# Kernel tuning notes

Hardware: AMD Instinct MI355X
Metric: run time of the kernel (lower is better)

## Reference

```python
import jax, jax.numpy as jnp
import numpy as np
import math
from jax import lax


def _conv(x, w, b, stride=1, pad=0, groups=1):
    # x: [B,C,H,W], w: [O, C//groups, kh, kw] (OIHW)
    out = lax.conv_general_dilated(x, w, (stride, stride), [(pad, pad), (pad, pad)],
                                   feature_group_count=groups,
                                   dimension_numbers=('NCHW', 'OIHW', 'NCHW'))
    return out + b.reshape(1, -1, 1, 1)


def _shared_conv(x, k2d, b, stride=1, pad=0):
    # SharedConv: one [k,k] kernel shared across all channels (depthwise), scalar bias
    C = x.shape[1]
    w = jnp.broadcast_to(k2d[None, None], (C, 1) + k2d.shape)
    out = lax.conv_general_dilated(x, w, (stride, stride), [(pad, pad), (pad, pad)],
                                   feature_group_count=C,
                                   dimension_numbers=('NCHW', 'OIHW', 'NCHW'))
    return out + b


def _bn(x, g, b, m, v, eps=1e-5):
    scale = (g / jnp.sqrt(v + eps)).reshape(1, -1, 1, 1)
    return (x - m.reshape(1, -1, 1, 1)) * scale + b.reshape(1, -1, 1, 1)


def _leaky(x, s=0.01):
    return jnp.where(x >= 0, x, s * x)


def _max_leaky(x, t, s):
    # cap values above threshold with leaky slope
    return jnp.where(x <= t, x, t + s * (x - t))


def _min_leaky(x, t, s):
    # cap values below threshold with leaky slope
    return jnp.where(x >= t, x, t + s * (x - t))


def _mode_pool(x, k=11, padding=1):
    # histogram mode pooling: 17 bins over quantized values, stride 1
    xp = jnp.pad(x, ((0, 0), (0, 0), (padding, padding), (padding, padding)))
    bins = jnp.clip(jnp.round(xp * 16.0), 0.0, 16.0).astype(jnp.int32)
    oh = jax.nn.one_hot(bins, 17, dtype=x.dtype)           # [B,C,Hp,Wp,17]
    counts = lax.reduce_window(oh, 0.0, lax.add, (1, 1, k, k, 1), (1, 1, 1, 1, 1), 'VALID')
    return jnp.argmax(counts, axis=-1).astype(x.dtype) / 16.0


def _emphase(x, w, k=11):
    # EmphaseLocal: unsharp-style local emphasis with per-channel learnable scale
    s = lax.reduce_window(x, 0.0, lax.add, (1, 1, k, k), (1, 1, 1, 1), 'SAME')
    avg = s / float(k * k)
    return x + w.reshape(1, -1, 1, 1) * (x - avg)


def setup_inputs() -> dict:
    key = jax.random.key(0)
    ks = jax.random.split(key, 20)
    f32 = jnp.float32
    B, Cin, H, W = 2, 3, 512, 512
    C2 = 64  # half_out_channels * 2
    return {
        'x': jax.random.uniform(ks[0], (B, Cin, H, W), f32),
        'w1': jax.random.normal(ks[1], (C2, Cin, 1, 1), f32) * 0.1,
        'b1': jax.random.normal(ks[2], (C2,), f32) * 0.05,
        'w2': jax.random.normal(ks[3], (C2, 2, 1, 1), f32) * 0.1,  # groups=32
        'b2': jax.random.normal(ks[4], (C2,), f32) * 0.05,
        'down_k': jax.random.normal(ks[5], (3, 3), f32) * 0.1,
        'down_b': jax.random.normal(ks[6], (), f32) * 0.05,
        'ft_gamma': 1.0 + jax.random.normal(ks[7], (C2,), f32) * 0.1,
        'ft_beta': jax.random.normal(ks[8], (C2,), f32) * 0.05,
        'ft_mean': jax.random.normal(ks[9], (C2,), f32) * 0.05,
        'ft_var': jax.random.uniform(ks[10], (C2,), f32, 0.5, 1.5),
        'ft_k': jax.random.normal(ks[11], (1, 1), f32) * 0.5 + 1.0,
        'ft_b': jax.random.normal(ks[12], (), f32) * 0.05,
        'emph_w': jax.random.normal(ks[13], (C2,), f32) * 0.1,
        'interp_k': jax.random.normal(ks[14], (5, 5), f32) * 0.1,
        'interp_b': jax.random.normal(ks[15], (), f32) * 0.05,
        'i_gamma': 1.0 + jax.random.normal(ks[16], (C2,), f32) * 0.1,
        'i_beta': jax.random.normal(ks[17], (C2,), f32) * 0.05,
        'i_mean': jax.random.normal(ks[18], (C2,), f32) * 0.05,
        'i_var': jax.random.uniform(ks[19], (C2,), f32, 0.5, 1.5),
    }


def reference(x, w1, b1, w2, b2, down_k, down_b,
              ft_gamma, ft_beta, ft_mean, ft_var, ft_k, ft_b, emph_w,
              interp_k, interp_b, i_gamma, i_beta, i_mean, i_var):
    B, _, H, W = x.shape
    C2 = w1.shape[0]
    # prepare: ColorDownsample(16) -> ModePool2d(11,1,1) -> 1x1 conv -> MaxLeakyReLU -> grouped 1x1 conv -> MinLeakyReLU
    xd = jnp.round(x * 255.0 / 16.0) * 16.0 / 256.0
    h = _mode_pool(xd, k=11, padding=1)                 # [B,Cin,H-8,W-8]
    h = _max_leaky(_conv(h, w1, b1), 0.1, 0.01)
    groups = C2 // w2.shape[1]
    d = _min_leaky(_conv(h, w2, b2, groups=groups), 0.1, 0.01)
    score = jnp.zeros((B, C2, H, W), x.dtype)
    n = math.floor(math.log(min(d.shape[2], d.shape[3]), 3))
    for _ in range(n):
        # downgrade: shared 3x3 stride-3 conv + leaky
        d = _leaky(_shared_conv(d, down_k, down_b, stride=3, pad=1))
        # zoom back to full resolution, then interpolate branch (shared 5x5 conv + BN + leaky)
        z = jax.image.resize(d, (B, C2, H, W), method='bilinear')
        z = _bn(_shared_conv(z, interp_k, interp_b, pad=2), i_gamma, i_beta, i_mean, i_var)
        score = score + _leaky(z)
    # ft applied 3 times with shared weights: BN -> shared 1x1 conv -> EmphaseLocal
    for _ in range(3):
        s = _bn(score, ft_gamma, ft_beta, ft_mean, ft_var)
        s = _shared_conv(s, ft_k, ft_b)
        score = _emphase(s, emph_w, k=11)
    return score
```

## Files before the change

### kernel.cpp

```cpp
#include <hip/hip_runtime.h>

#define NB 2
#define CIN 3
#define HH 512
#define WW 512
#define C2 64
#define HM 504

typedef float v2f  __attribute__((ext_vector_type(2)));
typedef float v2fu __attribute__((ext_vector_type(2), aligned(4)));

__global__ __launch_bounds__(256) void k_mode(const float* __restrict__ x,
                                              unsigned char* __restrict__ hmode) {
  __shared__ unsigned char tile[26 * 26];
  int bc  = blockIdx.z;
  int ty0 = blockIdx.y * 16, tx0 = blockIdx.x * 16;
  const float* src = x + (size_t)bc * HH * WW;
  for (int i = threadIdx.x; i < 26 * 26; i += 256) {
    int r = i / 26, cl = i % 26;
    int Y = ty0 + r, X = tx0 + cl;
    unsigned char v = 0;
    if (Y >= 1 && Y <= HH && X >= 1 && X <= WW) {
      float val = src[(Y - 1) * WW + (X - 1)];
      float q = rintf((val * 255.0f) / 16.0f);
      q = fminf(fmaxf(q, 0.0f), 16.0f);
      v = (unsigned char)(int)q;
    }
    tile[i] = v;
  }
  __syncthreads();
  int ty = threadIdx.x >> 4, tx = threadIdx.x & 15;
  int oy = ty0 + ty, ox = tx0 + tx;
  if (oy >= HM || ox >= HM) return;
  unsigned long long w0 = 0, w1 = 0, w2 = 0;
  for (int dy = 0; dy < 11; dy++) {
    #pragma unroll
    for (int dx = 0; dx < 11; dx++) {
      int b = tile[(ty + dy) * 26 + tx + dx];
      unsigned long long inc = 1ull << ((b & 7) * 8);
      if (b < 8) w0 += inc;
      else if (b < 16) w1 += inc;
      else w2 += inc;
    }
  }
  int best = -1, bestb = 0;
  #pragma unroll
  for (int b = 0; b < 17; b++) {
    int cnt;
    if (b < 8)       cnt = (int)((w0 >> (b * 8)) & 0xff);
    else if (b < 16) cnt = (int)((w1 >> ((b - 8) * 8)) & 0xff);
    else             cnt = (int)(w2 & 0xff);
    if (cnt > best) { best = cnt; bestb = b; }
  }
  hmode[bc * HM * HM + oy * HM + ox] = (unsigned char)bestb;
}

__global__ __launch_bounds__(256) void k_prepare(const unsigned char* __restrict__ hmode,
                                                 const float* __restrict__ w1,
                                                 const float* __restrict__ b1,
                                                 const float* __restrict__ w2,
                                                 const float* __restrict__ b2,
                                                 const float* __restrict__ down_k,
                                                 const float* __restrict__ down_b,
                                                 float* __restrict__ d1) {
  int bc = blockIdx.y;
  int b  = bc >> 6;
  int c  = bc & 63;
  int pix = blockIdx.x * 256 + threadIdx.x;
  if (pix >= 168 * 168) return;
  int oy = pix / 168, ox = pix % 168;
  int c0 = (c >> 1) << 1;
  float w1a0 = w1[c0 * 3], w1a1 = w1[c0 * 3 + 1], w1a2 = w1[c0 * 3 + 2], b1a = b1[c0];
  float w1b0 = w1[(c0 + 1) * 3], w1b1 = w1[(c0 + 1) * 3 + 1], w1b2 = w1[(c0 + 1) * 3 + 2], b1b = b1[c0 + 1];
  float w2a = w2[c * 2], w2b = w2[c * 2 + 1], b2c = b2[c];
  float kb = *down_b;
  const unsigned char* h0p = hmode + (b * 3 + 0) * HM * HM;
  const unsigned char* h1p = hmode + (b * 3 + 1) * HM * HM;
  const unsigned char* h2p = hmode + (b * 3 + 2) * HM * HM;
  float acc = 0.0f;
  #pragma unroll
  for (int ky = 0; ky < 3; ky++) {
    int y = 3 * oy - 1 + ky;
    if (y < 0 || y >= HM) continue;
    #pragma unroll
    for (int kx = 0; kx < 3; kx++) {
      int xx = 3 * ox - 1 + kx;
      if (xx < 0 || xx >= HM) continue;
      int o = y * HM + xx;
      float hh0 = h0p[o] * (1.0f / 16.0f);
      float hh1 = h1p[o] * (1.0f / 16.0f);
      float hh2 = h2p[o] * (1.0f / 16.0f);
      float a0 = w1a0 * hh0 + w1a1 * hh1 + w1a2 * hh2 + b1a;
      float a1 = w1b0 * hh0 + w1b1 * hh1 + w1b2 * hh2 + b1b;
      a0 = (a0 <= 0.1f) ? a0 : 0.1f + 0.01f * (a0 - 0.1f);
      a1 = (a1 <= 0.1f) ? a1 : 0.1f + 0.01f * (a1 - 0.1f);
      float v = w2a * a0 + w2b * a1 + b2c;
      v = (v >= 0.1f) ? v : 0.1f + 0.01f * (v - 0.1f);
      acc += down_k[ky * 3 + kx] * v;
    }
  }
  float r = acc + kb;
  r = (r >= 0.0f) ? r : 0.01f * r;
  d1[bc * 168 * 168 + pix] = r;
}

__global__ __launch_bounds__(256) void k_down(const float* __restrict__ din,
                                              float* __restrict__ dout,
                                              const float* __restrict__ down_k,
                                              const float* __restrict__ down_b,
                                              int S, int So) {
  int bc = blockIdx.y;
  int pix = blockIdx.x * 256 + threadIdx.x;
  if (pix >= So * So) return;
  int oy = pix / So, ox = pix % So;
  const float* p = din + bc * S * S;
  float acc = 0.0f;
  #pragma unroll
  for (int ky = 0; ky < 3; ky++) {
    int y = 3 * oy - 1 + ky;
    if (y < 0 || y >= S) continue;
    #pragma unroll
    for (int kx = 0; kx < 3; kx++) {
      int xx = 3 * ox - 1 + kx;
      if (xx < 0 || xx >= S) continue;
      acc += down_k[ky * 3 + kx] * p[y * S + xx];
    }
  }
  float r = acc + *down_b;
  r = (r >= 0.0f) ? r : 0.01f * r;
  dout[bc * So * So + pix] = r;
}

__global__ __launch_bounds__(256) void k_lut(float2* __restrict__ lutpk) {
  int idx = blockIdx.x * 256 + threadIdx.x;
  if (idx >= 5 * 512) return;
  int lvl = idx >> 9, Y = idx & 511;
  const int Ls[5] = {168, 56, 19, 7, 3};
  int L = Ls[lvl];
  float f = (Y + 0.5f) * ((float)L / 512.0f) - 0.5f;
  f = fminf(fmaxf(f, 0.0f), (float)(L - 1));
  int y0 = (int)f;
  float w = f - (float)y0;
  lutpk[idx] = make_float2(__int_as_float(y0), w);
}

#define XI(cc) ((cc) + ((((cc) >> 5)) << 2))
#define XSTR 148
__global__ __launch_bounds__(256, 4) void k_score(const float* __restrict__ d1,
                                                  const float* __restrict__ d2,
                                                  const float* __restrict__ d3,
                                                  const float* __restrict__ d4,
                                                  const float* __restrict__ d5,
                                                  const float2* __restrict__ lutpk,
                                                  const float* __restrict__ interp_k,
                                                  const float* __restrict__ interp_b,
                                                  const float* __restrict__ i_gamma,
                                                  const float* __restrict__ i_beta,
                                                  const float* __restrict__ i_mean,
                                                  const float* __restrict__ i_var,
                                                  float* __restrict__ score) {
  __shared__ float xrow[24 * XSTR];
  __shared__ float kap[64 * 36];
  __shared__ int   abase[64];

  int bc = blockIdx.y;
  int c  = bc & 63;
  int tile = blockIdx.x;
  int tyi = tile >> 2, txi = tile & 3;
  int ty0 = tyi * 64, tx0 = txi * 128;
  float K[25];
  #pragma unroll
  for (int i = 0; i < 25; i++)
    K[i] = __int_as_float(__builtin_amdgcn_readfirstlane(__float_as_int(interp_k[i])));
  float ib  = __int_as_float(__builtin_amdgcn_readfirstlane(__float_as_int(*interp_b)));
  float isc = i_gamma[c] * rsqrtf(i_var[c] + 1e-5f);
  float ibe = i_beta[c] - i_mean[c] * isc;
  int tid = threadIdx.x;
  int oyl = (tid >> 4) << 2, oxl = (tid & 15) << 3;
  const int pA = XI(oxl);
  const int pC = XI(oxl + 8);
  float acc[4][8];
  #pragma unroll
  for (int i = 0; i < 4; i++)
    #pragma unroll
    for (int j = 0; j < 8; j++) acc[i][j] = 0.0f;

  const float* dls[5] = {d1, d2, d3, d4, d5};
  const int Ls[5]  = {168, 56, 19, 7, 3};
  const int RLs[5] = {24, 10, 5, 3, 3};

  auto fillLevel = [&](int l) {
    int L = Ls[l], RR = RLs[l];
    const float* dp = dls[l] + bc * L * L;
    const float2* lp = lutpk + (l << 9);
    int Ylo = max(ty0 - 2, 0);
    int r0 = __float_as_int(lp[Ylo].x);
    {
      int y = tid >> 2, rr = tid & 3;
      int Y = ty0 + y;
      float kv0 = 0.0f, kv1 = 0.0f, kv2 = 0.0f, kv3 = 0.0f, kv4 = 0.0f;
      int ab = -1;
      #pragma unroll
      for (int ky = 0; ky < 5; ky++) {
        int yy = Y + ky - 2;
        if (yy >= 0 && yy < 512) {
          float2 pk = lp[yy];
          int a0 = __float_as_int(pk.x);
          float wv = pk.y;
          if (ab < 0) ab = a0;
          float cf = 0.0f;
          if (a0 - ab == rr)     cf += 1.0f - wv;
          if (a0 + 1 - ab == rr) cf += wv;
          kv0 += cf * K[ky * 5 + 0];
          kv1 += cf * K[ky * 5 + 1];
          kv2 += cf * K[ky * 5 + 2];
          kv3 += cf * K[ky * 5 + 3];
          kv4 += cf * K[ky * 5 + 4];
        }
      }
      float* kp = &kap[y * 36 + rr * 8];
      kp[0] = kv0; kp[1] = kv1; kp[2] = kv2; kp[3] = kv3; kp[4] = kv4;
      if (rr == 0) abase[y] = ab - r0;
    }
    for (int i = tid; i < RR * 132; i += 256) {
      int r = i / 132, xx = i - r * 132;
      int X = tx0 - 2 + xx;
      float v = 0.0f;
      if (X >= 0 && X < 512) {
        float2 pk = lp[X];
        int ix = __float_as_int(pk.x);
        float wx = pk.y;
        int gr = min(r0 + r, L - 1);
        const float* rp = dp + gr * L + ix;
        float v0 = rp[0], v1 = rp[1];
        v = v0 + wx * (v1 - v0);
      }
      xrow[r * XSTR + XI(xx)] = v;
    }
  };

  auto convAcc = [&](int rspan, int rlim) {
    int ab0 = abase[oyl];
    int ab1 = abase[oyl + 1];
    int ab2 = abase[oyl + 2];
    int ab3 = abase[oyl + 3];
    float t[4][8];
    #pragma unroll
    for (int i = 0; i < 4; i++)
      #pragma unroll
      for (int j = 0; j < 8; j++) t[i][j] = 0.0f;
    int gend = ab3 + rspan;
    for (int g = ab0; g < gend; ++g) {
      int row = min(g, rlim);
      const float* xp = &xrow[row * XSTR];
      float4 A = *(const float4*)(xp + pA);
      float4 B = *(const float4*)(xp + pA + 4);
      float4 Cx = *(const float4*)(xp + pC);
      float wnd[12] = {A.x, A.y, A.z, A.w, B.x, B.y, B.z, B.w, Cx.x, Cx.y, Cx.z, Cx.w};
      int abv[4] = {ab0, ab1, ab2, ab3};
      #pragma unroll
      for (int i = 0; i < 4; i++) {
        int rr = g - abv[i];
        if (rr >= 0 && rr < rspan) {
          const float* kp = &kap[(oyl + i) * 36 + rr * 8];
          float4 kk = *(const float4*)kp;
          float k4v = kp[4];
          #pragma unroll
          for (int j = 0; j < 8; j++)
            t[i][j] += kk.x * wnd[j] + kk.y * wnd[j + 1] + kk.z * wnd[j + 2] +
                       kk.w * wnd[j + 3] + k4v * wnd[j + 4];
        }
      }
    }
    #pragma unroll
    for (int i = 0; i < 4; i++)
      #pragma unroll
      for (int j = 0; j < 8; j++) {
        float v = (t[i][j] + ib) * isc + ibe;
        v = (v >= 0.0f) ? v : 0.01f * v;
        acc[i][j] += v;
      }
  };

  #pragma unroll 1
  for (int l = 0; l < 5; l++) {
    if (l) __syncthreads();
    fillLevel(l);
    __syncthreads();
    if (l == 0) convAcc(4, RLs[0] - 1);
    else        convAcc(3, RLs[l] - 1);
  }

  float* op = score + bc * 512 * 512;
  #pragma unroll
  for (int i = 0; i < 4; i++) {
    int Y = ty0 + oyl + i;
    float* orow = op + Y * 512 + tx0 + oxl;
    *(float4*)(orow)     = make_float4(acc[i][0], acc[i][1], acc[i][2], acc[i][3]);
    *(float4*)(orow + 4) = make_float4(acc[i][4], acc[i][5], acc[i][6], acc[i][7]);
  }
}

__global__ __launch_bounds__(256, 3) void k_ft_pipe(const float* __restrict__ s_in,
                                                    float* __restrict__ s_out,
                                                    const float* __restrict__ ft_gamma,
                                                    const float* __restrict__ ft_beta,
                                                    const float* __restrict__ ft_mean,
                                                    const float* __restrict__ ft_var,
                                                    const float* __restrict__ ft_k,
                                                    const float* __restrict__ ft_b,
                                                    const float* __restrict__ emph_w) {
  __shared__ float brow1[2][524];
  __shared__ float brow2[2][524];
  __shared__ float brow3[2][524];

  const int bc = blockIdx.y;
  const int c  = bc & 63;
  const int R0 = blockIdx.x << 7;
  const int mstart = R0 - 15;

  const float sc  = ft_gamma[c] * rsqrtf(ft_var[c] + 1e-5f);
  const float fk = *ft_k, fb = *ft_b;
  const float Aff = sc * fk;
  const float Cc  = (ft_beta[c] - ft_mean[c] * sc) * fk + fb;
  const float w   = emph_w[c];
  const float opw = 1.0f + w;
  const float okw = w * (1.0f / 121.0f);

  const int tid = threadIdx.x;
  const int x0  = tid << 1;

  const float* sp = s_in + ((size_t)bc << 18) + x0;
  float*       op = s_out + ((size_t)bc << 18) + x0;

  if (tid < 72) {
    int a = tid / 24, pb = (tid / 12) & 1, e = tid % 12;
    int idx = (e < 6) ? e : (512 + e);
    float* base = (a == 0) ? &brow1[pb][0] : (a == 1) ? &brow2[pb][0] : &brow3[pb][0];
    base[idx] = 0.0f;
  }

  auto ldraw = [&](int row) -> v2f {
    int rc = min(max(row, 0), 511);
    return *(const v2f*)(sp + ((size_t)rc << 9));
  };

  auto rowsum = [&](const float* b) -> v2f {
    const float* p = b + x0;
    v2f w0 = *(const v2f*)(p);
    v2f w1 = *(const v2f*)(p + 2);
    v2f w2 = *(const v2f*)(p + 4);
    v2f w3 = *(const v2f*)(p + 6);
    v2f w4 = *(const v2f*)(p + 8);
    v2f w5 = *(const v2f*)(p + 10);
    v2f w6 = *(const v2f*)(p + 12);
    float smid = ((w1.x + w1.y) + (w2.x + w2.y)) +
                 ((w3.x + w3.y) + (w4.x + w4.y)) + (w5.x + w5.y);
    v2f r;
    r.x = smid + w0.y;
    r.y = smid + w6.x;
    return r;
  };

  v2f cs1 = (v2f)0.0f, cs2 = (v2f)0.0f, cs3 = (v2f)0.0f;
  v2f out1p = (v2f)0.0f, out2p = (v2f)0.0f;

  v2f r2[12], r3[12];
  #pragma unroll
  for (int k = 0; k < 12; k++) { r2[k] = (v2f)0.0f; r3[k] = (v2f)0.0f; }

  v2f gf  = ldraw(mstart);
  v2f gfa = ldraw(mstart + 1);
  v2f go  = ldraw(mstart - 11);
  v2f gc  = ldraw(mstart - 5);

  #pragma unroll 1
  for (int ii = 0; ii < 14; ++ii) {
    #pragma unroll
    for (int j = 0; j < 12; ++j) {
      const int i = ii * 12 + j;
      const int m = mstart + i;
      v2f gf_n2 = ldraw(m + 2);
      v2f go_n  = ldraw(m - 10);
      v2f gc_n  = ldraw(m - 4);

      const int p = j & 1;

      {
        v2f u1f = (m >= 0 && m < 512) ? (gf * Aff + Cc) : (v2f)0.0f;
        int r = m - 11;
        v2f u1o = (r >= mstart && r >= 0 && r < 512) ? (go * Aff + Cc) : (v2f)0.0f;
        cs1 += u1f - u1o;
        *(v2f*)(&brow1[p][6 + x0]) = cs1;
      }
      {
        v2f u2s = out1p * Aff + Cc;
        v2f u2or = r2[(j + 1) % 12];
        r2[j] = u2s;
        int rf = m - 6;
        v2f u2f = (rf >= 0 && rf < 512) ? u2s : (v2f)0.0f;
        int r = m - 17;
        v2f u2o = (r >= mstart - 6 && r >= 0 && r < 512) ? u2or : (v2f)0.0f;
        cs2 += u2f - u2o;
        *(v2f*)(&brow2[p][6 + x0]) = cs2;
      }
      {
        v2f u3s = out2p * Aff + Cc;
        v2f u3or = r3[(j + 1) % 12];
        r3[j] = u3s;
        int rf = m - 12;
        v2f u3f = (rf >= 0 && rf < 512) ? u3s : (v2f)0.0f;
        int r = m - 23;
        v2f u3o = (r >= mstart - 12 && r >= 0 && r < 512) ? u3or : (v2f)0.0f;
        cs3 += u3f - u3o;
        *(v2f*)(&brow3[p][6 + x0]) = cs3;
      }
      __syncthreads();
      {
        int rc1 = m - 5;
        v2f u1c = (rc1 >= 0 && rc1 < 512) ? (gc * Aff + Cc) : (v2f)0.0f;
        v2f B1 = rowsum(&brow1[p][0]);
        out1p = u1c * opw - B1 * okw;
      }
      {
        int rc2 = m - 11;
        v2f u2cr = r2[(j + 7) % 12];
        v2f u2c = (rc2 >= mstart - 6 && rc2 >= 0 && rc2 < 512) ? u2cr : (v2f)0.0f;
        v2f B2 = rowsum(&brow2[p][0]);
        out2p = u2c * opw - B2 * okw;
      }
      {
        int rc3 = m - 17;
        v2f u3cr = r3[(j + 7) % 12];
        v2f u3c = (rc3 >= mstart - 12 && rc3 >= 0 && rc3 < 512) ? u3cr : (v2f)0.0f;
        v2f B3 = rowsum(&brow3[p][0]);
        v2f o3 = u3c * opw - B3 * okw;
        if (i >= 32 && i < 160)
          *(v2f*)(op + ((size_t)(m - 17) << 9)) = o3;
      }
      gf = gfa; gfa = gf_n2; go = go_n; gc = gc_n;
    }
  }
}

extern "C" void kernel_launch(void* const* d_in, const int* in_sizes, int n_in,
                              void* d_out, int out_size, void* d_ws, size_t ws_size,
                              hipStream_t stream) {
  const float* x        = (const float*)d_in[0];
  const float* w1       = (const float*)d_in[1];
  const float* b1       = (const float*)d_in[2];
  const float* w2       = (const float*)d_in[3];
  const float* b2       = (const float*)d_in[4];
  const float* down_k   = (const float*)d_in[5];
  const float* down_b   = (const float*)d_in[6];
  const float* ft_gamma = (const float*)d_in[7];
  const float* ft_beta  = (const float*)d_in[8];
  const float* ft_mean  = (const float*)d_in[9];
  const float* ft_var   = (const float*)d_in[10];
  const float* ft_k     = (const float*)d_in[11];
  const float* ft_b     = (const float*)d_in[12];
  const float* emph_w   = (const float*)d_in[13];
  const float* interp_k = (const float*)d_in[14];
  const float* interp_b = (const float*)d_in[15];
  const float* i_gamma  = (const float*)d_in[16];
  const float* i_beta   = (const float*)d_in[17];
  const float* i_mean   = (const float*)d_in[18];
  const float* i_var    = (const float*)d_in[19];
  float* out = (float*)d_out;

  char* ws = (char*)d_ws;
  size_t off = 0;
  auto alloc = [&](size_t bytes) { size_t r = off; off += (bytes + 255) & ~(size_t)255; return r; };
  unsigned char* hmode = (unsigned char*)(ws + alloc((size_t)NB * CIN * HM * HM));
  float* d1 = (float*)(ws + alloc((size_t)NB * C2 * 168 * 168 * 4));
  float* d2 = (float*)(ws + alloc((size_t)NB * C2 * 56 * 56 * 4));
  float* d3 = (float*)(ws + alloc((size_t)NB * C2 * 19 * 19 * 4));
  float* d4 = (float*)(ws + alloc((size_t)NB * C2 * 7 * 7 * 4));
  float* d5 = (float*)(ws + alloc((size_t)NB * C2 * 3 * 3 * 4));
  float* s0 = (float*)(ws + alloc((size_t)NB * C2 * 512 * 512 * 4));
  float2* lutpk = (float2*)(ws + alloc((size_t)5 * 512 * 8));

  k_mode<<<dim3(32, 32, NB * CIN), 256, 0, stream>>>(x, hmode);
  k_lut<<<10, 256, 0, stream>>>(lutpk);
  k_prepare<<<dim3((168 * 168 + 255) / 256, NB * C2), 256, 0, stream>>>(
      hmode, w1, b1, w2, b2, down_k, down_b, d1);
  k_down<<<dim3((56 * 56 + 255) / 256, NB * C2), 256, 0, stream>>>(d1, d2, down_k, down_b, 168, 56);
  k_down<<<dim3((19 * 19 + 255) / 256, NB * C2), 256, 0, stream>>>(d2, d3, down_k, down_b, 56, 19);
  k_down<<<dim3((7 * 7 + 255) / 256, NB * C2), 256, 0, stream>>>(d3, d4, down_k, down_b, 19, 7);
  k_down<<<dim3((3 * 3 + 255) / 256, NB * C2), 256, 0, stream>>>(d4, d5, down_k, down_b, 7, 3);
  k_score<<<dim3(32, NB * C2), 256, 0, stream>>>(d1, d2, d3, d4, d5, lutpk,
                                                 interp_k, interp_b,
                                                 i_gamma, i_beta, i_mean, i_var, s0);
  k_ft_pipe<<<dim3(4, NB * C2), 256, 0, stream>>>(s0, out, ft_gamma, ft_beta, ft_mean,
                                                  ft_var, ft_k, ft_b, emph_w);
}
```

Before: 542.0 us.

## Use sliding-window histogram for mode pooling with full-row tiles

Rewrites the mode-pool kernel so each block stages 14 full padded input rows in shared memory. Each thread computes 8 adjacent outputs along a row, updating its packed byte histogram by adding the incoming column and removing the outgoing one instead of recounting all 121 taps. The 8 results are written as a single 64-bit store. This cuts histogram work per output roughly fourfold and removes the overlapping halo loads of 16x16 tiles, but leaves each thread with a longer serial chain and launches fewer blocks.

```diff
diff --git a/kernel.cpp b/kernel.cpp
--- a/kernel.cpp
+++ b/kernel.cpp
@@ -12,47 +12,67 @@
 
 __global__ __launch_bounds__(256) void k_mode(const float* __restrict__ x,
                                               unsigned char* __restrict__ hmode) {
-  __shared__ unsigned char tile[26 * 26];
-  int bc  = blockIdx.z;
-  int ty0 = blockIdx.y * 16, tx0 = blockIdx.x * 16;
+  __shared__ unsigned char tile[14 * 520];
+  int bc  = blockIdx.y;
+  int ty0 = blockIdx.x * 4;
   const float* src = x + (size_t)bc * HH * WW;
-  for (int i = threadIdx.x; i < 26 * 26; i += 256) {
-    int r = i / 26, cl = i % 26;
-    int Y = ty0 + r, X = tx0 + cl;
-    unsigned char v = 0;
-    if (Y >= 1 && Y <= HH && X >= 1 && X <= WW) {
-      float val = src[(Y - 1) * WW + (X - 1)];
-      float q = rintf((val * 255.0f) / 16.0f);
-      q = fminf(fmaxf(q, 0.0f), 16.0f);
-      v = (unsigned char)(int)q;
-    }
-    tile[i] = v;
+  int tid = threadIdx.x;
+  for (int rr = 0; rr < 14; rr++) {
+    int Y = ty0 + rr;
+    for (int cl = tid; cl < 514; cl += 256) {
+      unsigned char v = 0;
+      if (Y >= 1 && Y <= HH && cl >= 1 && cl <= WW) {
+        float val = src[(Y - 1) * WW + (cl - 1)];
+        float q = rintf((val * 255.0f) / 16.0f);
+        q = fminf(fmaxf(q, 0.0f), 16.0f);
+        v = (unsigned char)(int)q;
+      }
+      tile[rr * 520 + cl] = v;
+    }
   }
   __syncthreads();
-  int ty = threadIdx.x >> 4, tx = threadIdx.x & 15;
-  int oy = ty0 + ty, ox = tx0 + tx;
-  if (oy >= HM || ox >= HM) return;
+  int r = tid >> 6, run = tid & 63;
+  int ox0 = run * 8;
+  if (ox0 >= HM) return;
+  int oy = ty0 + r;
   unsigned long long w0 = 0, w1 = 0, w2 = 0;
-  for (int dy = 0; dy < 11; dy++) {
-    #pragma unroll
-    for (int dx = 0; dx < 11; dx++) {
-      int b = tile[(ty + dy) * 26 + tx + dx];
-      unsigned long long inc = 1ull << ((b & 7) * 8);
-      if (b < 8) w0 += inc;
-      else if (b < 16) w1 += inc;
-      else w2 += inc;
-    }
-  }
-  int best = -1, bestb = 0;
-  #pragma unroll
-  for (int b = 0; b < 17; b++) {
-    int cnt;
-    if (b < 8)       cnt = (int)((w0 >> (b * 8)) & 0xff);
-    else if (b < 16) cnt = (int)((w1 >> ((b - 8) * 8)) & 0xff);
-    else             cnt = (int)(w2 & 0xff);
-    if (cnt > best) { best = cnt; bestb = b; }
-  }
-  hmode[bc * HM * HM + oy * HM + ox] = (unsigned char)bestb;
+  const unsigned char* tp = &tile[r * 520];
+  auto addb = [&](int b) {
+    unsigned long long inc = 1ull << ((b & 7) * 8);
+    if (b < 8) w0 += inc; else if (b < 16) w1 += inc; else w2 += inc;
+  };
+  auto subb = [&](int b) {
+    unsigned long long inc = 1ull << ((b & 7) * 8);
+    if (b < 8) w0 -= inc; else if (b < 16) w1 -= inc; else w2 -= inc;
+  };
+  #pragma unroll
+  for (int dy = 0; dy < 11; dy++)
+    #pragma unroll
+    for (int dx = 0; dx < 11; dx++)
+      addb(tp[dy * 520 + ox0 + dx]);
+  unsigned long long out64 = 0;
+  #pragma unroll
+  for (int k = 0; k < 8; k++) {
+    if (k > 0) {
+      int cadd = ox0 + k + 10, csub = ox0 + k - 1;
+      #pragma unroll
+      for (int dy = 0; dy < 11; dy++) {
+        addb(tp[dy * 520 + cadd]);
+        subb(tp[dy * 520 + csub]);
+      }
+    }
+    int best = -1, bestb = 0;
+    #pragma unroll
+    for (int b = 0; b < 17; b++) {
+      int cnt;
+      if (b < 8)       cnt = (int)((w0 >> (b * 8)) & 0xff);
+      else if (b < 16) cnt = (int)((w1 >> ((b - 8) * 8)) & 0xff);
+      else             cnt = (int)(w2 & 0xff);
+      if (cnt > best) { best = cnt; bestb = b; }
+    }
+    out64 |= (unsigned long long)bestb << (k * 8);
+  }
+  *(unsigned long long*)(hmode + (size_t)bc * HM * HM + oy * HM + ox0) = out64;
 }
 
 __global__ __launch_bounds__(256) void k_prepare(const unsigned char* __restrict__ hmode,
@@ -480,7 +500,7 @@
   float* s0 = (float*)(ws + alloc((size_t)NB * C2 * 512 * 512 * 4));
   float2* lutpk = (float2*)(ws + alloc((size_t)5 * 512 * 8));
 
-  k_mode<<<dim3(32, 32, NB * CIN), 256, 0, stream>>>(x, hmode);
+  k_mode<<<dim3(126, NB * CIN), 256, 0, stream>>>(x, hmode);
   k_lut<<<10, 256, 0, stream>>>(lutpk);
   k_prepare<<<dim3((168 * 168 + 255) / 256, NB * C2), 256, 0, stream>>>(
       hmode, w1, b1, w2, b2, down_k, down_b, d1);
```

After: 612.5 us. 13.0% more time.
